# Optimization experiments

Measured on AMD Instinct MI355X. Metric: run time of the kernel, lower is better.

The kernel has to match this reference:

```python
import jax, jax.numpy as jnp
import numpy as np

B, N, M, NF = 8, 512, 100, 42
DIMS = [NF, 256, 128, 64, 1]


def setup_inputs() -> dict:
    key = jax.random.key(0)
    ks = jax.random.split(key, 3 + len(DIMS) - 1)
    inp = {
        "image": jax.random.normal(ks[0], (B, N, NF), jnp.float32),
        "dfeat": jax.random.normal(ks[1], (B, N, M, NF, 3), jnp.float32) * 0.1,
        "neighbor": jax.random.randint(ks[2], (B, N, M), 0, N + 1),  # 0 = no neighbor, else 1-based atom idx
    }
    for l in range(len(DIMS) - 1):
        inp[f"W{l}"] = jax.random.normal(ks[3 + l], (DIMS[l], DIMS[l + 1]), jnp.float32) / np.sqrt(DIMS[l])
        inp[f"b{l}"] = jnp.zeros((DIMS[l + 1],), jnp.float32)
    return inp


def _atom_energy(x, Ws, bs):
    # per-atom MLP: sigmoid hidden layers, linear scalar output
    h = x
    for W, b in zip(Ws[:-1], bs[:-1]):
        h = jax.nn.sigmoid(h @ W + b)
    return (h @ Ws[-1] + bs[-1])[0]


def reference(image, dfeat, neighbor, W0, b0, W1, b1, W2, b2, W3, b3):
    Ws = (W0, W1, W2, W3)
    bs = (b0, b1, b2, b3)
    nb, na, nf = image.shape

    e_fn = lambda x: _atom_energy(x, Ws, bs)
    flat = image.reshape(-1, nf)
    Ei = jax.vmap(e_fn)(flat).reshape(nb, na)                      # [B, N]
    dE = jax.vmap(jax.grad(e_fn))(flat).reshape(nb, na, nf)        # dEi/dFeat, [B, N, F]
    Etot = jnp.sum(Ei, axis=1, keepdims=True)                      # [B, 1]

    # Force[b,i,:] = sum_m dE[b, neighbor[b,i,m]-1, :] @ dfeat[b,i,m,:,:], masking pad (0) entries
    mask = (neighbor > 0).astype(dE.dtype)                         # [B, N, M]
    idx = jnp.maximum(neighbor - 1, 0)                             # [B, N, M]
    dE_g = jax.vmap(lambda d, i: d[i])(dE, idx)                    # [B, N, M, F]
    Force = jnp.einsum('bnmf,bnmfd->bnd', dE_g * mask[..., None], dfeat)  # [B, N, 3]
    return Etot, Ei, Force
```

## Files before the change

kernel.cpp:

```cpp
#include <hip/hip_runtime.h>

#define NFEAT 42
#define H1 256
#define H2 128
#define H3 64
#define NB 8
#define NA 512
#define NM 100
#define TA 8

__device__ __forceinline__ float sigmoidf(float z) {
    return 1.0f / (1.0f + __expf(-z));
}

__global__ __launch_bounds__(256) void transpose_weights(
    const float* __restrict__ W0, const float* __restrict__ W1, const float* __restrict__ W2,
    float* __restrict__ W0T, float* __restrict__ W1T, float* __restrict__ W2T)
{
    int i = blockIdx.x * 256 + threadIdx.x;
    if (i < NFEAT * H1) {
        int f = i / H1, k = i - f * H1;
        W0T[k * NFEAT + f] = W0[i];
    }
    if (i < H1 * H2) {
        int k = i / H2, j = i - k * H2;
        W1T[j * H1 + k] = W1[i];
    }
    if (i < H2 * H3) {
        int j = i / H3, k = i - j * H3;
        W2T[k * H2 + j] = W2[i];
    }
}

__global__ __launch_bounds__(256) void mlp_fwd_bwd(
    const float* __restrict__ image,
    const float* __restrict__ W0, const float* __restrict__ b0,
    const float* __restrict__ W1, const float* __restrict__ b1,
    const float* __restrict__ W2, const float* __restrict__ b2,
    const float* __restrict__ W3, const float* __restrict__ b3,
    const float* __restrict__ W0T, const float* __restrict__ W1T, const float* __restrict__ W2T,
    float* __restrict__ Ei,
    float* __restrict__ dE)
{
    const int t = threadIdx.x;
    const int atom0 = blockIdx.x * TA;

    __shared__ float sx[TA][NFEAT];
    __shared__ __align__(16) float sh1[TA][H1];
    __shared__ __align__(16) float sh2[TA][H2];
    __shared__ __align__(16) float sh3[TA][H3];
    __shared__ __align__(16) float sd3[TA][H3];
    __shared__ __align__(16) float sd2[TA][H2];
    __shared__ __align__(16) float sd1[TA][H1];

    for (int i = t; i < TA * NFEAT; i += 256) {
        int a = i / NFEAT, f = i - a * NFEAT;
        sx[a][f] = image[(atom0 + a) * NFEAT + f];
    }
    __syncthreads();

    {
        float acc[TA];
        #pragma unroll
        for (int a = 0; a < TA; ++a) acc[a] = 0.f;
        for (int k = 0; k < NFEAT; ++k) {
            float w = W0[k * H1 + t];
            #pragma unroll
            for (int a = 0; a < TA; ++a) acc[a] += sx[a][k] * w;
        }
        float bb = b0[t];
        #pragma unroll
        for (int a = 0; a < TA; ++a) sh1[a][t] = sigmoidf(acc[a] + bb);
    }
    __syncthreads();

    {
        const int j = t & 127, g = t >> 7, a0 = g * 4;
        float acc[4] = {0.f, 0.f, 0.f, 0.f};
        for (int kk = 0; kk < H1 / 4; ++kk) {
            float w0_ = W1[(4 * kk + 0) * H2 + j];
            float w1_ = W1[(4 * kk + 1) * H2 + j];
            float w2_ = W1[(4 * kk + 2) * H2 + j];
            float w3_ = W1[(4 * kk + 3) * H2 + j];
            #pragma unroll
            for (int a = 0; a < 4; ++a) {
                float4 h = ((const float4*)sh1[a0 + a])[kk];
                acc[a] += h.x * w0_ + h.y * w1_ + h.z * w2_ + h.w * w3_;
            }
        }
        float bb = b1[j];
        #pragma unroll
        for (int a = 0; a < 4; ++a) sh2[a0 + a][j] = sigmoidf(acc[a] + bb);
    }
    __syncthreads();

    {
        const int j = t & 63, g = t >> 6, a0 = g * 2;
        float acc[2] = {0.f, 0.f};
        for (int kk = 0; kk < H2 / 4; ++kk) {
            float w0_ = W2[(4 * kk + 0) * H3 + j];
            float w1_ = W2[(4 * kk + 1) * H3 + j];
            float w2_ = W2[(4 * kk + 2) * H3 + j];
            float w3_ = W2[(4 * kk + 3) * H3 + j];
            #pragma unroll
            for (int a = 0; a < 2; ++a) {
                float4 h = ((const float4*)sh2[a0 + a])[kk];
                acc[a] += h.x * w0_ + h.y * w1_ + h.z * w2_ + h.w * w3_;
            }
        }
        float bb = b2[j];
        #pragma unroll
        for (int a = 0; a < 2; ++a) sh3[a0 + a][j] = sigmoidf(acc[a] + bb);
    }
    __syncthreads();

    {
        const int lane = t & 63, wv = t >> 6, a0 = wv * 2;
        float w = W3[lane];
        float bb = b3[0];
        #pragma unroll
        for (int a = a0; a < a0 + 2; ++a) {
            float h = sh3[a][lane];
            sd3[a][lane] = w * h * (1.f - h);
            float v = w * h;
            #pragma unroll
            for (int off = 32; off > 0; off >>= 1) v += __shfl_down(v, off, 64);
            if (lane == 0) Ei[atom0 + a] = v + bb;
        }
    }
    __syncthreads();

    {
        const int j = t & 127, g = t >> 7, a0 = g * 4;
        float acc[4] = {0.f, 0.f, 0.f, 0.f};
        for (int kk = 0; kk < H3 / 4; ++kk) {
            float w0_ = W2T[(4 * kk + 0) * H2 + j];
            float w1_ = W2T[(4 * kk + 1) * H2 + j];
            float w2_ = W2T[(4 * kk + 2) * H2 + j];
            float w3_ = W2T[(4 * kk + 3) * H2 + j];
            #pragma unroll
            for (int a = 0; a < 4; ++a) {
                float4 d = ((const float4*)sd3[a0 + a])[kk];
                acc[a] += d.x * w0_ + d.y * w1_ + d.z * w2_ + d.w * w3_;
            }
        }
        #pragma unroll
        for (int a = 0; a < 4; ++a) {
            float h = sh2[a0 + a][j];
            sd2[a0 + a][j] = acc[a] * h * (1.f - h);
        }
    }
    __syncthreads();

    {
        float acc[TA];
        #pragma unroll
        for (int a = 0; a < TA; ++a) acc[a] = 0.f;
        for (int jj = 0; jj < H2 / 4; ++jj) {
            float w0_ = W1T[(4 * jj + 0) * H1 + t];
            float w1_ = W1T[(4 * jj + 1) * H1 + t];
            float w2_ = W1T[(4 * jj + 2) * H1 + t];
            float w3_ = W1T[(4 * jj + 3) * H1 + t];
            #pragma unroll
            for (int a = 0; a < TA; ++a) {
                float4 d = ((const float4*)sd2[a])[jj];
                acc[a] += d.x * w0_ + d.y * w1_ + d.z * w2_ + d.w * w3_;
            }
        }
        #pragma unroll
        for (int a = 0; a < TA; ++a) {
            float h = sh1[a][t];
            sd1[a][t] = acc[a] * h * (1.f - h);
        }
    }
    __syncthreads();

    {
        const int f = t & 63, g = t >> 6, a0 = g * 2;
        if (f < NFEAT) {
            float acc[2] = {0.f, 0.f};
            for (int kk = 0; kk < H1 / 4; ++kk) {
                float w0_ = W0T[(4 * kk + 0) * NFEAT + f];
                float w1_ = W0T[(4 * kk + 1) * NFEAT + f];
                float w2_ = W0T[(4 * kk + 2) * NFEAT + f];
                float w3_ = W0T[(4 * kk + 3) * NFEAT + f];
                #pragma unroll
                for (int a = 0; a < 2; ++a) {
                    float4 d = ((const float4*)sd1[a0 + a])[kk];
                    acc[a] += d.x * w0_ + d.y * w1_ + d.z * w2_ + d.w * w3_;
                }
            }
            #pragma unroll
            for (int a = 0; a < 2; ++a)
                dE[(atom0 + a0 + a) * NFEAT + f] = acc[a];
        }
    }
}

__global__ __launch_bounds__(256) void etot_kernel(const float* __restrict__ Ei,
                                                   float* __restrict__ Etot)
{
    const int b = blockIdx.x;
    const int t = threadIdx.x;
    float v = Ei[b * NA + t] + Ei[b * NA + t + 256];
    __shared__ float red[4];
    #pragma unroll
    for (int off = 32; off > 0; off >>= 1) v += __shfl_down(v, off, 64);
    if ((t & 63) == 0) red[t >> 6] = v;
    __syncthreads();
    if (t == 0) Etot[b] = red[0] + red[1] + red[2] + red[3];
}

__global__ __launch_bounds__(256) void force_kernel(
    const float* __restrict__ dfeat,
    const int*   __restrict__ neighbor,
    const float* __restrict__ dE,
    float* __restrict__ Force)
{
    const int bi = blockIdx.x;
    const int b  = bi >> 9;
    const int t  = threadIdx.x;

    __shared__ int   s_nb[NM];
    __shared__ float s_dE[104 * NFEAT];
    __shared__ float s_part[1008];
    __shared__ float s_red[126];

    if (t < NM) s_nb[t] = neighbor[bi * NM + t];
    for (int i = t; i < 4 * NFEAT; i += 256) s_dE[NM * NFEAT + i] = 0.f;
    __syncthreads();

    for (int i = t; i < NM * NFEAT; i += 256) {
        int m = i / NFEAT, f = i - m * NFEAT;
        int n = s_nb[m];
        s_dE[i] = (n > 0) ? dE[((b << 9) + n - 1) * NFEAT + f] : 0.f;
    }
    __syncthreads();

    if (t < 252) {
        const int e4 = 4 * t;
        int off[4];
        #pragma unroll
        for (int c = 0; c < 4; ++c) {
            int ee = e4 + c;
            int r  = ee / 126;
            int e  = ee - r * 126;
            off[c] = r * NFEAT + e / 3;
        }
        const float* base = dfeat + (size_t)bi * (NM * NFEAT * 3);
        float acc[4] = {0.f, 0.f, 0.f, 0.f};

        for (int m0 = 0; m0 < 96; m0 += 8) {
            float4 v = *(const float4*)(base + m0 * 126 + e4);
            const float* sd = s_dE + m0 * NFEAT;
            acc[0] += v.x * sd[off[0]];
            acc[1] += v.y * sd[off[1]];
            acc[2] += v.z * sd[off[2]];
            acc[3] += v.w * sd[off[3]];
        }
        {
            const int m0 = 96;
            float vv[4];
            if (bi != NB * NA - 1) {
                float4 v = *(const float4*)(base + m0 * 126 + e4);
                vv[0] = v.x; vv[1] = v.y; vv[2] = v.z; vv[3] = v.w;
            } else {
                #pragma unroll
                for (int c = 0; c < 4; ++c) {
                    int r = (e4 + c) / 126;
                    vv[c] = (m0 + r < NM) ? base[m0 * 126 + e4 + c] : 0.f;
                }
            }
            const float* sd = s_dE + m0 * NFEAT;
            #pragma unroll
            for (int c = 0; c < 4; ++c) acc[c] += vv[c] * sd[off[c]];
        }
        #pragma unroll
        for (int c = 0; c < 4; ++c) s_part[e4 + c] = acc[c];
    }
    __syncthreads();

    if (t < 126) {
        float s = 0.f;
        #pragma unroll
        for (int r = 0; r < 8; ++r) s += s_part[r * 126 + t];
        s_red[t] = s;
    }
    __syncthreads();

    if (t < 3) {
        float s = 0.f;
        #pragma unroll
        for (int f = 0; f < NFEAT; ++f) s += s_red[f * 3 + t];
        Force[bi * 3 + t] = s;
    }
}

extern "C" void kernel_launch(void* const* d_in, const int* in_sizes, int n_in,
                              void* d_out, int out_size, void* d_ws, size_t ws_size,
                              hipStream_t stream) {
    const float* image    = (const float*)d_in[0];
    const float* dfeat    = (const float*)d_in[1];
    const int*   neighbor = (const int*)  d_in[2];
    const float* W0 = (const float*)d_in[3];
    const float* b0 = (const float*)d_in[4];
    const float* W1 = (const float*)d_in[5];
    const float* b1 = (const float*)d_in[6];
    const float* W2 = (const float*)d_in[7];
    const float* b2 = (const float*)d_in[8];
    const float* W3 = (const float*)d_in[9];
    const float* b3 = (const float*)d_in[10];

    float* out   = (float*)d_out;
    float* Etot  = out;
    float* Ei    = out + NB;
    float* Force = out + NB + NB * NA;

    float* dE  = (float*)d_ws;
    float* W0T = dE  + NB * NA * NFEAT;
    float* W1T = W0T + NFEAT * H1;
    float* W2T = W1T + H1 * H2;

    transpose_weights<<<(H1 * H2 + 255) / 256, 256, 0, stream>>>(W0, W1, W2, W0T, W1T, W2T);
    mlp_fwd_bwd<<<(NB * NA) / TA, 256, 0, stream>>>(image, W0, b0, W1, b1, W2, b2, W3, b3,
                                                    W0T, W1T, W2T, Ei, dE);
    etot_kernel<<<NB, 256, 0, stream>>>(Ei, Etot);
    force_kernel<<<NB * NA, 256, 0, stream>>>(dfeat, neighbor, dE, Force);
}
```

Measured before the change: 343.0 us.

## Prefetch dfeat into registers before gather; vectorize MLP weight reads per thread

The force kernel now issues all thirteen float4 dfeat loads per thread before the neighbor index load and dE gather, so HBM latency overlaps the shared-memory staging. The MLP kernel halves atoms per block and stores weights so each thread reads a contiguous row as float4, with the feature dim padded to 44. This raises register use in the force kernel and doubles the MLP block count and weight re-reads.

```diff
diff --git a/kernel.cpp b/kernel.cpp
--- a/kernel.cpp
+++ b/kernel.cpp
@@ -1,13 +1,14 @@
 #include <hip/hip_runtime.h>
 
 #define NFEAT 42
+#define NF_PAD 44
 #define H1 256
 #define H2 128
 #define H3 64
 #define NB 8
 #define NA 512
 #define NM 100
-#define TA 8
+#define TA 4
 
 __device__ __forceinline__ float sigmoidf(float z) {
     return 1.0f / (1.0f + __expf(-z));
@@ -18,17 +19,17 @@
     float* __restrict__ W0T, float* __restrict__ W1T, float* __restrict__ W2T)
 {
     int i = blockIdx.x * 256 + threadIdx.x;
-    if (i < NFEAT * H1) {
-        int f = i / H1, k = i - f * H1;
-        W0T[k * NFEAT + f] = W0[i];
-    }
-    if (i < H1 * H2) {
-        int k = i / H2, j = i - k * H2;
-        W1T[j * H1 + k] = W1[i];
-    }
-    if (i < H2 * H3) {
-        int j = i / H3, k = i - j * H3;
-        W2T[k * H2 + j] = W2[i];
+    if (i < H1 * NF_PAD) {
+        int k = i / NF_PAD, f = i - k * NF_PAD;
+        W0T[i] = (f < NFEAT) ? W0[f * H1 + k] : 0.f;
+    }
+    if (i < H2 * H1) {
+        int j = i >> 8, k = i & 255;
+        W1T[i] = W1[k * H2 + j];
+    }
+    if (i < H3 * H2) {
+        int j = i >> 7, k = i & 127;
+        W2T[i] = W2[k * H3 + j];
     }
 }
 
@@ -45,7 +46,7 @@
     const int t = threadIdx.x;
     const int atom0 = blockIdx.x * TA;
 
-    __shared__ float sx[TA][NFEAT];
+    __shared__ __align__(16) float sx[TA][NF_PAD];
     __shared__ __align__(16) float sh1[TA][H1];
     __shared__ __align__(16) float sh2[TA][H2];
     __shared__ __align__(16) float sh3[TA][H3];
@@ -53,20 +54,23 @@
     __shared__ __align__(16) float sd2[TA][H2];
     __shared__ __align__(16) float sd1[TA][H1];
 
-    for (int i = t; i < TA * NFEAT; i += 256) {
-        int a = i / NFEAT, f = i - a * NFEAT;
-        sx[a][f] = image[(atom0 + a) * NFEAT + f];
-    }
-    __syncthreads();
-
-    {
-        float acc[TA];
-        #pragma unroll
-        for (int a = 0; a < TA; ++a) acc[a] = 0.f;
-        for (int k = 0; k < NFEAT; ++k) {
-            float w = W0[k * H1 + t];
-            #pragma unroll
-            for (int a = 0; a < TA; ++a) acc[a] += sx[a][k] * w;
+    for (int i = t; i < TA * NF_PAD; i += 256) {
+        int a = i / NF_PAD, f = i - a * NF_PAD;
+        sx[a][f] = (f < NFEAT) ? image[(atom0 + a) * NFEAT + f] : 0.f;
+    }
+    __syncthreads();
+
+    {
+        float acc[TA] = {0.f, 0.f, 0.f, 0.f};
+        const float4* wp = (const float4*)(W0T + t * NF_PAD);
+        #pragma unroll
+        for (int c = 0; c < NF_PAD / 4; ++c) {
+            float4 w = wp[c];
+            #pragma unroll
+            for (int a = 0; a < TA; ++a) {
+                float4 x = ((const float4*)sx[a])[c];
+                acc[a] += w.x * x.x + w.y * x.y + w.z * x.z + w.w * x.w;
+            }
         }
         float bb = b0[t];
         #pragma unroll
@@ -75,77 +79,65 @@
     __syncthreads();
 
     {
-        const int j = t & 127, g = t >> 7, a0 = g * 4;
-        float acc[4] = {0.f, 0.f, 0.f, 0.f};
+        const int j = t & 127, a0 = (t >> 7) * 2;
+        float acc[2] = {0.f, 0.f};
+        const float4* wp = (const float4*)(W1T + j * H1);
+        #pragma unroll 8
         for (int kk = 0; kk < H1 / 4; ++kk) {
-            float w0_ = W1[(4 * kk + 0) * H2 + j];
-            float w1_ = W1[(4 * kk + 1) * H2 + j];
-            float w2_ = W1[(4 * kk + 2) * H2 + j];
-            float w3_ = W1[(4 * kk + 3) * H2 + j];
-            #pragma unroll
-            for (int a = 0; a < 4; ++a) {
+            float4 w = wp[kk];
+            #pragma unroll
+            for (int a = 0; a < 2; ++a) {
                 float4 h = ((const float4*)sh1[a0 + a])[kk];
-                acc[a] += h.x * w0_ + h.y * w1_ + h.z * w2_ + h.w * w3_;
+                acc[a] += w.x * h.x + w.y * h.y + w.z * h.z + w.w * h.w;
             }
         }
         float bb = b1[j];
         #pragma unroll
-        for (int a = 0; a < 4; ++a) sh2[a0 + a][j] = sigmoidf(acc[a] + bb);
-    }
-    __syncthreads();
-
-    {
-        const int j = t & 63, g = t >> 6, a0 = g * 2;
+        for (int a = 0; a < 2; ++a) sh2[a0 + a][j] = sigmoidf(acc[a] + bb);
+    }
+    __syncthreads();
+
+    {
+        const int j = t & 63, a = t >> 6;
+        float acc = 0.f;
+        const float4* wp = (const float4*)(W2T + j * H2);
+        #pragma unroll 8
+        for (int kk = 0; kk < H2 / 4; ++kk) {
+            float4 w = wp[kk];
+            float4 h = ((const float4*)sh2[a])[kk];
+            acc += w.x * h.x + w.y * h.y + w.z * h.z + w.w * h.w;
+        }
+        sh3[a][j] = sigmoidf(acc + b2[j]);
+    }
+    __syncthreads();
+
+    {
+        const int lane = t & 63, a = t >> 6;
+        float w = W3[lane];
+        float h = sh3[a][lane];
+        sd3[a][lane] = w * h * (1.f - h);
+        float v = w * h;
+        #pragma unroll
+        for (int off = 32; off > 0; off >>= 1) v += __shfl_down(v, off, 64);
+        if (lane == 0) Ei[atom0 + a] = v + b3[0];
+    }
+    __syncthreads();
+
+    {
+        const int j = t & 127, a0 = (t >> 7) * 2;
         float acc[2] = {0.f, 0.f};
-        for (int kk = 0; kk < H2 / 4; ++kk) {
-            float w0_ = W2[(4 * kk + 0) * H3 + j];
-            float w1_ = W2[(4 * kk + 1) * H3 + j];
-            float w2_ = W2[(4 * kk + 2) * H3 + j];
-            float w3_ = W2[(4 * kk + 3) * H3 + j];
+        const float4* wp = (const float4*)(W2 + j * H3);
+        #pragma unroll
+        for (int kk = 0; kk < H3 / 4; ++kk) {
+            float4 w = wp[kk];
             #pragma unroll
             for (int a = 0; a < 2; ++a) {
-                float4 h = ((const float4*)sh2[a0 + a])[kk];
-                acc[a] += h.x * w0_ + h.y * w1_ + h.z * w2_ + h.w * w3_;
-            }
-        }
-        float bb = b2[j];
-        #pragma unroll
-        for (int a = 0; a < 2; ++a) sh3[a0 + a][j] = sigmoidf(acc[a] + bb);
-    }
-    __syncthreads();
-
-    {
-        const int lane = t & 63, wv = t >> 6, a0 = wv * 2;
-        float w = W3[lane];
-        float bb = b3[0];
-        #pragma unroll
-        for (int a = a0; a < a0 + 2; ++a) {
-            float h = sh3[a][lane];
-            sd3[a][lane] = w * h * (1.f - h);
-            float v = w * h;
-            #pragma unroll
-            for (int off = 32; off > 0; off >>= 1) v += __shfl_down(v, off, 64);
-            if (lane == 0) Ei[atom0 + a] = v + bb;
-        }
-    }
-    __syncthreads();
-
-    {
-        const int j = t & 127, g = t >> 7, a0 = g * 4;
-        float acc[4] = {0.f, 0.f, 0.f, 0.f};
-        for (int kk = 0; kk < H3 / 4; ++kk) {
-            float w0_ = W2T[(4 * kk + 0) * H2 + j];
-            float w1_ = W2T[(4 * kk + 1) * H2 + j];
-            float w2_ = W2T[(4 * kk + 2) * H2 + j];
-            float w3_ = W2T[(4 * kk + 3) * H2 + j];
-            #pragma unroll
-            for (int a = 0; a < 4; ++a) {
                 float4 d = ((const float4*)sd3[a0 + a])[kk];
-                acc[a] += d.x * w0_ + d.y * w1_ + d.z * w2_ + d.w * w3_;
-            }
-        }
-        #pragma unroll
-        for (int a = 0; a < 4; ++a) {
+                acc[a] += w.x * d.x + w.y * d.y + w.z * d.z + w.w * d.w;
+            }
+        }
+        #pragma unroll
+        for (int a = 0; a < 2; ++a) {
             float h = sh2[a0 + a][j];
             sd2[a0 + a][j] = acc[a] * h * (1.f - h);
         }
@@ -153,18 +145,15 @@
     __syncthreads();
 
     {
-        float acc[TA];
-        #pragma unroll
-        for (int a = 0; a < TA; ++a) acc[a] = 0.f;
+        float acc[TA] = {0.f, 0.f, 0.f, 0.f};
+        const float4* wp = (const float4*)(W1 + t * H2);
+        #pragma unroll 4
         for (int jj = 0; jj < H2 / 4; ++jj) {
-            float w0_ = W1T[(4 * jj + 0) * H1 + t];
-            float w1_ = W1T[(4 * jj + 1) * H1 + t];
-            float w2_ = W1T[(4 * jj + 2) * H1 + t];
-            float w3_ = W1T[(4 * jj + 3) * H1 + t];
+            float4 w = wp[jj];
             #pragma unroll
             for (int a = 0; a < TA; ++a) {
                 float4 d = ((const float4*)sd2[a])[jj];
-                acc[a] += d.x * w0_ + d.y * w1_ + d.z * w2_ + d.w * w3_;
+                acc[a] += w.x * d.x + w.y * d.y + w.z * d.z + w.w * d.w;
             }
         }
         #pragma unroll
@@ -176,23 +165,17 @@
     __syncthreads();
 
     {
-        const int f = t & 63, g = t >> 6, a0 = g * 2;
+        const int f = t & 63, a = t >> 6;
         if (f < NFEAT) {
-            float acc[2] = {0.f, 0.f};
+            float acc = 0.f;
+            const float4* wp = (const float4*)(W0 + f * H1);
+            #pragma unroll 8
             for (int kk = 0; kk < H1 / 4; ++kk) {
-                float w0_ = W0T[(4 * kk + 0) * NFEAT + f];
-                float w1_ = W0T[(4 * kk + 1) * NFEAT + f];
-                float w2_ = W0T[(4 * kk + 2) * NFEAT + f];
-                float w3_ = W0T[(4 * kk + 3) * NFEAT + f];
-                #pragma unroll
-                for (int a = 0; a < 2; ++a) {
-                    float4 d = ((const float4*)sd1[a0 + a])[kk];
-                    acc[a] += d.x * w0_ + d.y * w1_ + d.z * w2_ + d.w * w3_;
-                }
-            }
-            #pragma unroll
-            for (int a = 0; a < 2; ++a)
-                dE[(atom0 + a0 + a) * NFEAT + f] = acc[a];
+                float4 w = wp[kk];
+                float4 d = ((const float4*)sd1[a])[kk];
+                acc += w.x * d.x + w.y * d.y + w.z * d.z + w.w * d.w;
+            }
+            dE[(atom0 + a) * NFEAT + f] = acc;
         }
     }
 }
@@ -226,6 +209,24 @@
     __shared__ float s_part[1008];
     __shared__ float s_red[126];
 
+    float4 v[13];
+    if (t < 252) {
+        const float* base = dfeat + (size_t)bi * (NM * NFEAT * 3) + 4 * t;
+        #pragma unroll
+        for (int r = 0; r < 12; ++r) v[r] = *(const float4*)(base + r * 1008);
+        if (bi != NB * NA - 1) {
+            v[12] = *(const float4*)(base + 12 * 1008);
+        } else {
+            float vv[4];
+            #pragma unroll
+            for (int c = 0; c < 4; ++c) {
+                int r = (4 * t + c) / 126;
+                vv[c] = (96 + r < NM) ? base[12 * 1008 + c] : 0.f;
+            }
+            v[12] = make_float4(vv[0], vv[1], vv[2], vv[3]);
+        }
+    }
+
     if (t < NM) s_nb[t] = neighbor[bi * NM + t];
     for (int i = t; i < 4 * NFEAT; i += 256) s_dE[NM * NFEAT + i] = 0.f;
     __syncthreads();
@@ -247,33 +248,14 @@
             int e  = ee - r * 126;
             off[c] = r * NFEAT + e / 3;
         }
-        const float* base = dfeat + (size_t)bi * (NM * NFEAT * 3);
         float acc[4] = {0.f, 0.f, 0.f, 0.f};
-
-        for (int m0 = 0; m0 < 96; m0 += 8) {
-            float4 v = *(const float4*)(base + m0 * 126 + e4);
-            const float* sd = s_dE + m0 * NFEAT;
-            acc[0] += v.x * sd[off[0]];
-            acc[1] += v.y * sd[off[1]];
-            acc[2] += v.z * sd[off[2]];
-            acc[3] += v.w * sd[off[3]];
-        }
-        {
-            const int m0 = 96;
-            float vv[4];
-            if (bi != NB * NA - 1) {
-                float4 v = *(const float4*)(base + m0 * 126 + e4);
-                vv[0] = v.x; vv[1] = v.y; vv[2] = v.z; vv[3] = v.w;
-            } else {
-                #pragma unroll
-                for (int c = 0; c < 4; ++c) {
-                    int r = (e4 + c) / 126;
-                    vv[c] = (m0 + r < NM) ? base[m0 * 126 + e4 + c] : 0.f;
-                }
-            }
-            const float* sd = s_dE + m0 * NFEAT;
-            #pragma unroll
-            for (int c = 0; c < 4; ++c) acc[c] += vv[c] * sd[off[c]];
+        #pragma unroll
+        for (int g = 0; g < 13; ++g) {
+            const float* sd = s_dE + g * 8 * NFEAT;
+            acc[0] += v[g].x * sd[off[0]];
+            acc[1] += v[g].y * sd[off[1]];
+            acc[2] += v[g].z * sd[off[2]];
+            acc[3] += v[g].w * sd[off[3]];
         }
         #pragma unroll
         for (int c = 0; c < 4; ++c) s_part[e4 + c] = acc[c];
@@ -318,7 +300,7 @@
 
     float* dE  = (float*)d_ws;
     float* W0T = dE  + NB * NA * NFEAT;
-    float* W1T = W0T + NFEAT * H1;
+    float* W1T = W0T + H1 * NF_PAD;
     float* W2T = W1T + H1 * H2;
 
     transpose_weights<<<(H1 * H2 + 255) / 256, 256, 0, stream>>>(W0, W1, W2, W0T, W1T, W2T);
```

New measurement: 400.7 us. 16.8% more time.

## Fuse all four kernels into one cooperative kernel with grid syncs

Applied to the files above, without the earlier changes.

Replaces the separate transpose, MLP forward/backward, energy-sum and force kernels with a single cooperative launch of 512 blocks, separated by grid-wide barriers. Each block transposes a slice of the weights, runs the MLP for 8 atoms, and then computes forces for 8 atoms in a loop. The aim is to remove three kernel-launch gaps. In exchange it adds grid.sync costs, and the force phase now runs 512 blocks serially over 8 atoms each instead of 4096 independent blocks, which may reduce the latency hiding available for the large dfeat stream.

```diff
diff --git a/kernel.cpp b/kernel.cpp
--- a/kernel.cpp
+++ b/kernel.cpp
@@ -1,4 +1,7 @@
 #include <hip/hip_runtime.h>
+#include <hip/hip_cooperative_groups.h>
+
+namespace cg = cooperative_groups;
 
 #define NFEAT 42
 #define H1 256
@@ -8,42 +11,27 @@
 #define NA 512
 #define NM 100
 #define TA 8
+#define NBLK 512
 
 __device__ __forceinline__ float sigmoidf(float z) {
     return 1.0f / (1.0f + __expf(-z));
 }
 
-__global__ __launch_bounds__(256) void transpose_weights(
-    const float* __restrict__ W0, const float* __restrict__ W1, const float* __restrict__ W2,
-    float* __restrict__ W0T, float* __restrict__ W1T, float* __restrict__ W2T)
-{
-    int i = blockIdx.x * 256 + threadIdx.x;
-    if (i < NFEAT * H1) {
-        int f = i / H1, k = i - f * H1;
-        W0T[k * NFEAT + f] = W0[i];
-    }
-    if (i < H1 * H2) {
-        int k = i / H2, j = i - k * H2;
-        W1T[j * H1 + k] = W1[i];
-    }
-    if (i < H2 * H3) {
-        int j = i / H3, k = i - j * H3;
-        W2T[k * H2 + j] = W2[i];
-    }
-}
-
-__global__ __launch_bounds__(256) void mlp_fwd_bwd(
+__global__ __launch_bounds__(256) void fused_all(
     const float* __restrict__ image,
+    const float* __restrict__ dfeat,
+    const int*   __restrict__ neighbor,
     const float* __restrict__ W0, const float* __restrict__ b0,
     const float* __restrict__ W1, const float* __restrict__ b1,
     const float* __restrict__ W2, const float* __restrict__ b2,
     const float* __restrict__ W3, const float* __restrict__ b3,
-    const float* __restrict__ W0T, const float* __restrict__ W1T, const float* __restrict__ W2T,
-    float* __restrict__ Ei,
+    float* __restrict__ W0T, float* __restrict__ W1T, float* __restrict__ W2T,
+    float* __restrict__ Etot, float* __restrict__ Ei, float* __restrict__ Force,
     float* __restrict__ dE)
 {
-    const int t = threadIdx.x;
-    const int atom0 = blockIdx.x * TA;
+    const int t   = threadIdx.x;
+    const int blk = blockIdx.x;
+    cg::grid_group grid = cg::this_grid();
 
     __shared__ float sx[TA][NFEAT];
     __shared__ __align__(16) float sh1[TA][H1];
@@ -52,247 +40,262 @@
     __shared__ __align__(16) float sd3[TA][H3];
     __shared__ __align__(16) float sd2[TA][H2];
     __shared__ __align__(16) float sd1[TA][H1];
-
-    for (int i = t; i < TA * NFEAT; i += 256) {
-        int a = i / NFEAT, f = i - a * NFEAT;
-        sx[a][f] = image[(atom0 + a) * NFEAT + f];
-    }
-    __syncthreads();
-
-    {
-        float acc[TA];
-        #pragma unroll
-        for (int a = 0; a < TA; ++a) acc[a] = 0.f;
-        for (int k = 0; k < NFEAT; ++k) {
-            float w = W0[k * H1 + t];
-            #pragma unroll
-            for (int a = 0; a < TA; ++a) acc[a] += sx[a][k] * w;
-        }
-        float bb = b0[t];
-        #pragma unroll
-        for (int a = 0; a < TA; ++a) sh1[a][t] = sigmoidf(acc[a] + bb);
-    }
-    __syncthreads();
-
-    {
-        const int j = t & 127, g = t >> 7, a0 = g * 4;
-        float acc[4] = {0.f, 0.f, 0.f, 0.f};
-        for (int kk = 0; kk < H1 / 4; ++kk) {
-            float w0_ = W1[(4 * kk + 0) * H2 + j];
-            float w1_ = W1[(4 * kk + 1) * H2 + j];
-            float w2_ = W1[(4 * kk + 2) * H2 + j];
-            float w3_ = W1[(4 * kk + 3) * H2 + j];
-            #pragma unroll
-            for (int a = 0; a < 4; ++a) {
-                float4 h = ((const float4*)sh1[a0 + a])[kk];
-                acc[a] += h.x * w0_ + h.y * w1_ + h.z * w2_ + h.w * w3_;
-            }
-        }
-        float bb = b1[j];
-        #pragma unroll
-        for (int a = 0; a < 4; ++a) sh2[a0 + a][j] = sigmoidf(acc[a] + bb);
-    }
-    __syncthreads();
-
-    {
-        const int j = t & 63, g = t >> 6, a0 = g * 2;
-        float acc[2] = {0.f, 0.f};
-        for (int kk = 0; kk < H2 / 4; ++kk) {
-            float w0_ = W2[(4 * kk + 0) * H3 + j];
-            float w1_ = W2[(4 * kk + 1) * H3 + j];
-            float w2_ = W2[(4 * kk + 2) * H3 + j];
-            float w3_ = W2[(4 * kk + 3) * H3 + j];
-            #pragma unroll
-            for (int a = 0; a < 2; ++a) {
-                float4 h = ((const float4*)sh2[a0 + a])[kk];
-                acc[a] += h.x * w0_ + h.y * w1_ + h.z * w2_ + h.w * w3_;
-            }
-        }
-        float bb = b2[j];
-        #pragma unroll
-        for (int a = 0; a < 2; ++a) sh3[a0 + a][j] = sigmoidf(acc[a] + bb);
-    }
-    __syncthreads();
-
-    {
-        const int lane = t & 63, wv = t >> 6, a0 = wv * 2;
-        float w = W3[lane];
-        float bb = b3[0];
-        #pragma unroll
-        for (int a = a0; a < a0 + 2; ++a) {
-            float h = sh3[a][lane];
-            sd3[a][lane] = w * h * (1.f - h);
-            float v = w * h;
-            #pragma unroll
-            for (int off = 32; off > 0; off >>= 1) v += __shfl_down(v, off, 64);
-            if (lane == 0) Ei[atom0 + a] = v + bb;
-        }
-    }
-    __syncthreads();
-
-    {
-        const int j = t & 127, g = t >> 7, a0 = g * 4;
-        float acc[4] = {0.f, 0.f, 0.f, 0.f};
-        for (int kk = 0; kk < H3 / 4; ++kk) {
-            float w0_ = W2T[(4 * kk + 0) * H2 + j];
-            float w1_ = W2T[(4 * kk + 1) * H2 + j];
-            float w2_ = W2T[(4 * kk + 2) * H2 + j];
-            float w3_ = W2T[(4 * kk + 3) * H2 + j];
-            #pragma unroll
-            for (int a = 0; a < 4; ++a) {
-                float4 d = ((const float4*)sd3[a0 + a])[kk];
-                acc[a] += d.x * w0_ + d.y * w1_ + d.z * w2_ + d.w * w3_;
-            }
-        }
-        #pragma unroll
-        for (int a = 0; a < 4; ++a) {
-            float h = sh2[a0 + a][j];
-            sd2[a0 + a][j] = acc[a] * h * (1.f - h);
-        }
-    }
-    __syncthreads();
-
-    {
-        float acc[TA];
-        #pragma unroll
-        for (int a = 0; a < TA; ++a) acc[a] = 0.f;
-        for (int jj = 0; jj < H2 / 4; ++jj) {
-            float w0_ = W1T[(4 * jj + 0) * H1 + t];
-            float w1_ = W1T[(4 * jj + 1) * H1 + t];
-            float w2_ = W1T[(4 * jj + 2) * H1 + t];
-            float w3_ = W1T[(4 * jj + 3) * H1 + t];
-            #pragma unroll
-            for (int a = 0; a < TA; ++a) {
-                float4 d = ((const float4*)sd2[a])[jj];
-                acc[a] += d.x * w0_ + d.y * w1_ + d.z * w2_ + d.w * w3_;
-            }
-        }
-        #pragma unroll
-        for (int a = 0; a < TA; ++a) {
-            float h = sh1[a][t];
-            sd1[a][t] = acc[a] * h * (1.f - h);
-        }
-    }
-    __syncthreads();
-
-    {
-        const int f = t & 63, g = t >> 6, a0 = g * 2;
-        if (f < NFEAT) {
-            float acc[2] = {0.f, 0.f};
-            for (int kk = 0; kk < H1 / 4; ++kk) {
-                float w0_ = W0T[(4 * kk + 0) * NFEAT + f];
-                float w1_ = W0T[(4 * kk + 1) * NFEAT + f];
-                float w2_ = W0T[(4 * kk + 2) * NFEAT + f];
-                float w3_ = W0T[(4 * kk + 3) * NFEAT + f];
-                #pragma unroll
-                for (int a = 0; a < 2; ++a) {
-                    float4 d = ((const float4*)sd1[a0 + a])[kk];
-                    acc[a] += d.x * w0_ + d.y * w1_ + d.z * w2_ + d.w * w3_;
-                }
-            }
-            #pragma unroll
-            for (int a = 0; a < 2; ++a)
-                dE[(atom0 + a0 + a) * NFEAT + f] = acc[a];
-        }
-    }
-}
-
-__global__ __launch_bounds__(256) void etot_kernel(const float* __restrict__ Ei,
-                                                   float* __restrict__ Etot)
-{
-    const int b = blockIdx.x;
-    const int t = threadIdx.x;
-    float v = Ei[b * NA + t] + Ei[b * NA + t + 256];
-    __shared__ float red[4];
-    #pragma unroll
-    for (int off = 32; off > 0; off >>= 1) v += __shfl_down(v, off, 64);
-    if ((t & 63) == 0) red[t >> 6] = v;
-    __syncthreads();
-    if (t == 0) Etot[b] = red[0] + red[1] + red[2] + red[3];
-}
-
-__global__ __launch_bounds__(256) void force_kernel(
-    const float* __restrict__ dfeat,
-    const int*   __restrict__ neighbor,
-    const float* __restrict__ dE,
-    float* __restrict__ Force)
-{
-    const int bi = blockIdx.x;
-    const int b  = bi >> 9;
-    const int t  = threadIdx.x;
-
     __shared__ int   s_nb[NM];
     __shared__ float s_dE[104 * NFEAT];
     __shared__ float s_part[1008];
     __shared__ float s_red[126];
 
-    if (t < NM) s_nb[t] = neighbor[bi * NM + t];
+    {
+        int i = blk * 256 + t;
+        if (i < NFEAT * H1) {
+            int f = i / H1, k = i - f * H1;
+            W0T[k * NFEAT + f] = W0[i];
+        }
+        if (i < H1 * H2) {
+            int k = i / H2, j = i - k * H2;
+            W1T[j * H1 + k] = W1[i];
+        }
+        if (i < H2 * H3) {
+            int j = i / H3, k = i - j * H3;
+            W2T[k * H2 + j] = W2[i];
+        }
+    }
+    __threadfence();
+    grid.sync();
+
+    {
+        const int atom0 = blk * TA;
+
+        for (int i = t; i < TA * NFEAT; i += 256) {
+            int a = i / NFEAT, f = i - a * NFEAT;
+            sx[a][f] = image[(atom0 + a) * NFEAT + f];
+        }
+        __syncthreads();
+
+        {
+            float acc[TA];
+            #pragma unroll
+            for (int a = 0; a < TA; ++a) acc[a] = 0.f;
+            for (int k = 0; k < NFEAT; ++k) {
+                float w = W0[k * H1 + t];
+                #pragma unroll
+                for (int a = 0; a < TA; ++a) acc[a] += sx[a][k] * w;
+            }
+            float bb = b0[t];
+            #pragma unroll
+            for (int a = 0; a < TA; ++a) sh1[a][t] = sigmoidf(acc[a] + bb);
+        }
+        __syncthreads();
+
+        {
+            const int j = t & 127, g = t >> 7, a0 = g * 4;
+            float acc[4] = {0.f, 0.f, 0.f, 0.f};
+            for (int kk = 0; kk < H1 / 4; ++kk) {
+                float w0_ = W1[(4 * kk + 0) * H2 + j];
+                float w1_ = W1[(4 * kk + 1) * H2 + j];
+                float w2_ = W1[(4 * kk + 2) * H2 + j];
+                float w3_ = W1[(4 * kk + 3) * H2 + j];
+                #pragma unroll
+                for (int a = 0; a < 4; ++a) {
+                    float4 h = ((const float4*)sh1[a0 + a])[kk];
+                    acc[a] += h.x * w0_ + h.y * w1_ + h.z * w2_ + h.w * w3_;
+                }
+            }
+            float bb = b1[j];
+            #pragma unroll
+            for (int a = 0; a < 4; ++a) sh2[a0 + a][j] = sigmoidf(acc[a] + bb);
+        }
+        __syncthreads();
+
+        {
+            const int j = t & 63, g = t >> 6, a0 = g * 2;
+            float acc[2] = {0.f, 0.f};
+            for (int kk = 0; kk < H2 / 4; ++kk) {
+                float w0_ = W2[(4 * kk + 0) * H3 + j];
+                float w1_ = W2[(4 * kk + 1) * H3 + j];
+                float w2_ = W2[(4 * kk + 2) * H3 + j];
+                float w3_ = W2[(4 * kk + 3) * H3 + j];
+                #pragma unroll
+                for (int a = 0; a < 2; ++a) {
+                    float4 h = ((const float4*)sh2[a0 + a])[kk];
+                    acc[a] += h.x * w0_ + h.y * w1_ + h.z * w2_ + h.w * w3_;
+                }
+            }
+            float bb = b2[j];
+            #pragma unroll
+            for (int a = 0; a < 2; ++a) sh3[a0 + a][j] = sigmoidf(acc[a] + bb);
+        }
+        __syncthreads();
+
+        {
+            const int lane = t & 63, wv = t >> 6, a0 = wv * 2;
+            float w = W3[lane];
+            float bb = b3[0];
+            #pragma unroll
+            for (int a = a0; a < a0 + 2; ++a) {
+                float h = sh3[a][lane];
+                sd3[a][lane] = w * h * (1.f - h);
+                float v = w * h;
+                #pragma unroll
+                for (int off = 32; off > 0; off >>= 1) v += __shfl_down(v, off, 64);
+                if (lane == 0) Ei[atom0 + a] = v + bb;
+            }
+        }
+        __syncthreads();
+
+        {
+            const int j = t & 127, g = t >> 7, a0 = g * 4;
+            float acc[4] = {0.f, 0.f, 0.f, 0.f};
+            for (int kk = 0; kk < H3 / 4; ++kk) {
+                float w0_ = W2T[(4 * kk + 0) * H2 + j];
+                float w1_ = W2T[(4 * kk + 1) * H2 + j];
+                float w2_ = W2T[(4 * kk + 2) * H2 + j];
+                float w3_ = W2T[(4 * kk + 3) * H2 + j];
+                #pragma unroll
+                for (int a = 0; a < 4; ++a) {
+                    float4 d = ((const float4*)sd3[a0 + a])[kk];
+                    acc[a] += d.x * w0_ + d.y * w1_ + d.z * w2_ + d.w * w3_;
+                }
+            }
+            #pragma unroll
+            for (int a = 0; a < 4; ++a) {
+                float h = sh2[a0 + a][j];
+                sd2[a0 + a][j] = acc[a] * h * (1.f - h);
+            }
+        }
+        __syncthreads();
+
+        {
+            float acc[TA];
+            #pragma unroll
+            for (int a = 0; a < TA; ++a) acc[a] = 0.f;
+            for (int jj = 0; jj < H2 / 4; ++jj) {
+                float w0_ = W1T[(4 * jj + 0) * H1 + t];
+                float w1_ = W1T[(4 * jj + 1) * H1 + t];
+                float w2_ = W1T[(4 * jj + 2) * H1 + t];
+                float w3_ = W1T[(4 * jj + 3) * H1 + t];
+                #pragma unroll
+                for (int a = 0; a < TA; ++a) {
+                    float4 d = ((const float4*)sd2[a])[jj];
+                    acc[a] += d.x * w0_ + d.y * w1_ + d.z * w2_ + d.w * w3_;
+                }
+            }
+            #pragma unroll
+            for (int a = 0; a < TA; ++a) {
+                float h = sh1[a][t];
+                sd1[a][t] = acc[a] * h * (1.f - h);
+            }
+        }
+        __syncthreads();
+
+        {
+            const int f = t & 63, g = t >> 6, a0 = g * 2;
+            if (f < NFEAT) {
+                float acc[2] = {0.f, 0.f};
+                for (int kk = 0; kk < H1 / 4; ++kk) {
+                    float w0_ = W0T[(4 * kk + 0) * NFEAT + f];
+                    float w1_ = W0T[(4 * kk + 1) * NFEAT + f];
+                    float w2_ = W0T[(4 * kk + 2) * NFEAT + f];
+                    float w3_ = W0T[(4 * kk + 3) * NFEAT + f];
+                    #pragma unroll
+                    for (int a = 0; a < 2; ++a) {
+                        float4 d = ((const float4*)sd1[a0 + a])[kk];
+                        acc[a] += d.x * w0_ + d.y * w1_ + d.z * w2_ + d.w * w3_;
+                    }
+                }
+                #pragma unroll
+                for (int a = 0; a < 2; ++a)
+                    dE[(atom0 + a0 + a) * NFEAT + f] = acc[a];
+            }
+        }
+    }
+    __threadfence();
+    grid.sync();
+
+    if (blk < NB) {
+        float v = Ei[blk * NA + t] + Ei[blk * NA + t + 256];
+        #pragma unroll
+        for (int off = 32; off > 0; off >>= 1) v += __shfl_down(v, off, 64);
+        if ((t & 63) == 0) s_red[t >> 6] = v;
+        __syncthreads();
+        if (t == 0) Etot[blk] = s_red[0] + s_red[1] + s_red[2] + s_red[3];
+        __syncthreads();
+    }
+
     for (int i = t; i < 4 * NFEAT; i += 256) s_dE[NM * NFEAT + i] = 0.f;
-    __syncthreads();
-
-    for (int i = t; i < NM * NFEAT; i += 256) {
-        int m = i / NFEAT, f = i - m * NFEAT;
-        int n = s_nb[m];
-        s_dE[i] = (n > 0) ? dE[((b << 9) + n - 1) * NFEAT + f] : 0.f;
-    }
-    __syncthreads();
-
-    if (t < 252) {
-        const int e4 = 4 * t;
-        int off[4];
-        #pragma unroll
-        for (int c = 0; c < 4; ++c) {
-            int ee = e4 + c;
-            int r  = ee / 126;
-            int e  = ee - r * 126;
-            off[c] = r * NFEAT + e / 3;
-        }
-        const float* base = dfeat + (size_t)bi * (NM * NFEAT * 3);
-        float acc[4] = {0.f, 0.f, 0.f, 0.f};
-
-        for (int m0 = 0; m0 < 96; m0 += 8) {
-            float4 v = *(const float4*)(base + m0 * 126 + e4);
-            const float* sd = s_dE + m0 * NFEAT;
-            acc[0] += v.x * sd[off[0]];
-            acc[1] += v.y * sd[off[1]];
-            acc[2] += v.z * sd[off[2]];
-            acc[3] += v.w * sd[off[3]];
-        }
-        {
-            const int m0 = 96;
-            float vv[4];
-            if (bi != NB * NA - 1) {
+
+    for (int k8 = 0; k8 < 8; ++k8) {
+        const int bi = blk * 8 + k8;
+        const int b  = bi >> 9;
+
+        if (t < NM) s_nb[t] = neighbor[bi * NM + t];
+        __syncthreads();
+
+        for (int i = t; i < NM * NFEAT; i += 256) {
+            int m = i / NFEAT, f = i - m * NFEAT;
+            int n = s_nb[m];
+            s_dE[i] = (n > 0) ? dE[((b << 9) + n - 1) * NFEAT + f] : 0.f;
+        }
+        __syncthreads();
+
+        if (t < 252) {
+            const int e4 = 4 * t;
+            int off[4];
+            #pragma unroll
+            for (int c = 0; c < 4; ++c) {
+                int ee = e4 + c;
+                int r  = ee / 126;
+                int e  = ee - r * 126;
+                off[c] = r * NFEAT + e / 3;
+            }
+            const float* base = dfeat + (size_t)bi * (NM * NFEAT * 3);
+            float acc[4] = {0.f, 0.f, 0.f, 0.f};
+
+            for (int m0 = 0; m0 < 96; m0 += 8) {
                 float4 v = *(const float4*)(base + m0 * 126 + e4);
-                vv[0] = v.x; vv[1] = v.y; vv[2] = v.z; vv[3] = v.w;
-            } else {
-                #pragma unroll
-                for (int c = 0; c < 4; ++c) {
-                    int r = (e4 + c) / 126;
-                    vv[c] = (m0 + r < NM) ? base[m0 * 126 + e4 + c] : 0.f;
-                }
-            }
-            const float* sd = s_dE + m0 * NFEAT;
-            #pragma unroll
-            for (int c = 0; c < 4; ++c) acc[c] += vv[c] * sd[off[c]];
-        }
-        #pragma unroll
-        for (int c = 0; c < 4; ++c) s_part[e4 + c] = acc[c];
-    }
-    __syncthreads();
-
-    if (t < 126) {
-        float s = 0.f;
-        #pragma unroll
-        for (int r = 0; r < 8; ++r) s += s_part[r * 126 + t];
-        s_red[t] = s;
-    }
-    __syncthreads();
-
-    if (t < 3) {
-        float s = 0.f;
-        #pragma unroll
-        for (int f = 0; f < NFEAT; ++f) s += s_red[f * 3 + t];
-        Force[bi * 3 + t] = s;
+                const float* sd = s_dE + m0 * NFEAT;
+                acc[0] += v.x * sd[off[0]];
+                acc[1] += v.y * sd[off[1]];
+                acc[2] += v.z * sd[off[2]];
+                acc[3] += v.w * sd[off[3]];
+            }
+            {
+                const int m0 = 96;
+                float vv[4];
+                if (bi != NB * NA - 1) {
+                    float4 v = *(const float4*)(base + m0 * 126 + e4);
+                    vv[0] = v.x; vv[1] = v.y; vv[2] = v.z; vv[3] = v.w;
+                } else {
+                    #pragma unroll
+                    for (int c = 0; c < 4; ++c) {
+                        int r = (e4 + c) / 126;
+                        vv[c] = (m0 + r < NM) ? base[m0 * 126 + e4 + c] : 0.f;
+                    }
+                }
+                const float* sd = s_dE + m0 * NFEAT;
+                #pragma unroll
+                for (int c = 0; c < 4; ++c) acc[c] += vv[c] * sd[off[c]];
+            }
+            #pragma unroll
+            for (int c = 0; c < 4; ++c) s_part[e4 + c] = acc[c];
+        }
+        __syncthreads();
+
+        if (t < 126) {
+            float s = 0.f;
+            #pragma unroll
+            for (int r = 0; r < 8; ++r) s += s_part[r * 126 + t];
+            s_red[t] = s;
+        }
+        __syncthreads();
+
+        if (t < 3) {
+            float s = 0.f;
+            #pragma unroll
+            for (int f = 0; f < NFEAT; ++f) s += s_red[f * 3 + t];
+            Force[bi * 3 + t] = s;
+        }
+        __syncthreads();
     }
 }
 
@@ -321,9 +324,13 @@
     float* W1T = W0T + NFEAT * H1;
     float* W2T = W1T + H1 * H2;
 
-    transpose_weights<<<(H1 * H2 + 255) / 256, 256, 0, stream>>>(W0, W1, W2, W0T, W1T, W2T);
-    mlp_fwd_bwd<<<(NB * NA) / TA, 256, 0, stream>>>(image, W0, b0, W1, b1, W2, b2, W3, b3,
-                                                    W0T, W1T, W2T, Ei, dE);
-    etot_kernel<<<NB, 256, 0, stream>>>(Ei, Etot);
-    force_kernel<<<NB * NA, 256, 0, stream>>>(dfeat, neighbor, dE, Force);
+    void* kargs[] = {
+        (void*)&image, (void*)&dfeat, (void*)&neighbor,
+        (void*)&W0, (void*)&b0, (void*)&W1, (void*)&b1,
+        (void*)&W2, (void*)&b2, (void*)&W3, (void*)&b3,
+        (void*)&W0T, (void*)&W1T, (void*)&W2T,
+        (void*)&Etot, (void*)&Ei, (void*)&Force, (void*)&dE
+    };
+    hipLaunchCooperativeKernel((const void*)fused_all, dim3(NBLK), dim3(256),
+                               kargs, 0, stream);
 }
```

Measured after the change: 582.4 us. +69.8%, slower.

## Split force work per atom across two blocks and fuse Etot reduction

Applied to the files above, without the earlier changes.

Each atom's force computation is split across two blocks, each covering about half of the 100 neighbors. Partial results are combined with atomicAdd into a Force buffer that the weight-transpose kernel now zeroes. The Etot reduction is folded into the first blocks of the force kernel, removing a separate launch. This doubles the block count and cuts shared memory per block to raise occupancy and parallelism on the bandwidth-bound dfeat stream, at the cost of atomics and a duplicated neighbor-gather setup per block.

```diff
diff --git a/kernel.cpp b/kernel.cpp
--- a/kernel.cpp
+++ b/kernel.cpp
@@ -15,7 +15,8 @@
 
 __global__ __launch_bounds__(256) void transpose_weights(
     const float* __restrict__ W0, const float* __restrict__ W1, const float* __restrict__ W2,
-    float* __restrict__ W0T, float* __restrict__ W1T, float* __restrict__ W2T)
+    float* __restrict__ W0T, float* __restrict__ W1T, float* __restrict__ W2T,
+    float* __restrict__ Force)
 {
     int i = blockIdx.x * 256 + threadIdx.x;
     if (i < NFEAT * H1) {
@@ -30,6 +31,7 @@
         int j = i / H3, k = i - j * H3;
         W2T[k * H2 + j] = W2[i];
     }
+    if (i < NB * NA * 3) Force[i] = 0.f;
 }
 
 __global__ __launch_bounds__(256) void mlp_fwd_bwd(
@@ -197,40 +199,45 @@
     }
 }
 
-__global__ __launch_bounds__(256) void etot_kernel(const float* __restrict__ Ei,
-                                                   float* __restrict__ Etot)
-{
-    const int b = blockIdx.x;
-    const int t = threadIdx.x;
-    float v = Ei[b * NA + t] + Ei[b * NA + t + 256];
-    __shared__ float red[4];
-    #pragma unroll
-    for (int off = 32; off > 0; off >>= 1) v += __shfl_down(v, off, 64);
-    if ((t & 63) == 0) red[t >> 6] = v;
-    __syncthreads();
-    if (t == 0) Etot[b] = red[0] + red[1] + red[2] + red[3];
-}
-
-__global__ __launch_bounds__(256) void force_kernel(
+__global__ __launch_bounds__(256) void force_etot_kernel(
     const float* __restrict__ dfeat,
     const int*   __restrict__ neighbor,
     const float* __restrict__ dE,
+    const float* __restrict__ Ei,
+    float* __restrict__ Etot,
     float* __restrict__ Force)
 {
-    const int bi = blockIdx.x;
-    const int b  = bi >> 9;
-    const int t  = threadIdx.x;
-
-    __shared__ int   s_nb[NM];
-    __shared__ float s_dE[104 * NFEAT];
+    const int blk  = blockIdx.x;
+    const int bi   = blk >> 1;
+    const int half = blk & 1;
+    const int b    = bi >> 9;
+    const int t    = threadIdx.x;
+
+    __shared__ int   s_nb[56];
+    __shared__ float s_dE[56 * NFEAT];
     __shared__ float s_part[1008];
     __shared__ float s_red[126];
-
-    if (t < NM) s_nb[t] = neighbor[bi * NM + t];
-    for (int i = t; i < 4 * NFEAT; i += 256) s_dE[NM * NFEAT + i] = 0.f;
-    __syncthreads();
-
-    for (int i = t; i < NM * NFEAT; i += 256) {
+    __shared__ float e_red[4];
+
+    if (blk < NB) {
+        float v = Ei[blk * NA + t] + Ei[blk * NA + t + 256];
+        #pragma unroll
+        for (int off = 32; off > 0; off >>= 1) v += __shfl_down(v, off, 64);
+        if ((t & 63) == 0) e_red[t >> 6] = v;
+        __syncthreads();
+        if (t == 0) Etot[blk] = e_red[0] + e_red[1] + e_red[2] + e_red[3];
+    }
+
+    const int g0   = half ? 7 : 0;
+    const int ng   = half ? 6 : 7;
+    const int r0   = g0 * 8;
+    const int nrow = half ? 44 : 56;
+
+    if (t < nrow) s_nb[t] = neighbor[bi * NM + r0 + t];
+    for (int i = nrow * NFEAT + t; i < 8 * ng * NFEAT; i += 256) s_dE[i] = 0.f;
+    __syncthreads();
+
+    for (int i = t; i < nrow * NFEAT; i += 256) {
         int m = i / NFEAT, f = i - m * NFEAT;
         int n = s_nb[m];
         s_dE[i] = (n > 0) ? dE[((b << 9) + n - 1) * NFEAT + f] : 0.f;
@@ -249,29 +256,29 @@
         }
         const float* base = dfeat + (size_t)bi * (NM * NFEAT * 3);
         float acc[4] = {0.f, 0.f, 0.f, 0.f};
-
-        for (int m0 = 0; m0 < 96; m0 += 8) {
-            float4 v = *(const float4*)(base + m0 * 126 + e4);
-            const float* sd = s_dE + m0 * NFEAT;
+        const int glast = g0 + ng - 1;
+
+        for (int g = g0; g < glast; ++g) {
+            float4 v = *(const float4*)(base + g * 1008 + e4);
+            const float* sd = s_dE + (g - g0) * 8 * NFEAT;
             acc[0] += v.x * sd[off[0]];
             acc[1] += v.y * sd[off[1]];
             acc[2] += v.z * sd[off[2]];
             acc[3] += v.w * sd[off[3]];
         }
         {
-            const int m0 = 96;
             float vv[4];
-            if (bi != NB * NA - 1) {
-                float4 v = *(const float4*)(base + m0 * 126 + e4);
+            if (!(half && bi == NB * NA - 1)) {
+                float4 v = *(const float4*)(base + glast * 1008 + e4);
                 vv[0] = v.x; vv[1] = v.y; vv[2] = v.z; vv[3] = v.w;
             } else {
                 #pragma unroll
                 for (int c = 0; c < 4; ++c) {
                     int r = (e4 + c) / 126;
-                    vv[c] = (m0 + r < NM) ? base[m0 * 126 + e4 + c] : 0.f;
+                    vv[c] = (96 + r < NM) ? base[glast * 1008 + e4 + c] : 0.f;
                 }
             }
-            const float* sd = s_dE + m0 * NFEAT;
+            const float* sd = s_dE + (glast - g0) * 8 * NFEAT;
             #pragma unroll
             for (int c = 0; c < 4; ++c) acc[c] += vv[c] * sd[off[c]];
         }
@@ -292,7 +299,7 @@
         float s = 0.f;
         #pragma unroll
         for (int f = 0; f < NFEAT; ++f) s += s_red[f * 3 + t];
-        Force[bi * 3 + t] = s;
+        atomicAdd(&Force[bi * 3 + t], s);
     }
 }
 
@@ -321,9 +328,8 @@
     float* W1T = W0T + NFEAT * H1;
     float* W2T = W1T + H1 * H2;
 
-    transpose_weights<<<(H1 * H2 + 255) / 256, 256, 0, stream>>>(W0, W1, W2, W0T, W1T, W2T);
+    transpose_weights<<<(H1 * H2 + 255) / 256, 256, 0, stream>>>(W0, W1, W2, W0T, W1T, W2T, Force);
     mlp_fwd_bwd<<<(NB * NA) / TA, 256, 0, stream>>>(image, W0, b0, W1, b1, W2, b2, W3, b3,
                                                     W0T, W1T, W2T, Ei, dE);
-    etot_kernel<<<NB, 256, 0, stream>>>(Ei, Etot);
-    force_kernel<<<NB * NA, 256, 0, stream>>>(dfeat, neighbor, dE, Force);
-}
+    force_etot_kernel<<<2 * NB * NA, 256, 0, stream>>>(dfeat, neighbor, dE, Ei, Etot, Force);
+}
```

Result: no change. 343.3 us (+0.1%).
